# Performance work log

Hardware: AMD Instinct MI355X
Metric: run time of the kernel (lower is better)

The kernel has to match this reference:

```python
import jax, jax.numpy as jnp
import numpy as np

NEG_SLOPE = 0.2  # PyG GATv2Conv default negative_slope
NUM_GRAPHS = 512


def _gatv2_layer(x, Wl, Wr, att, bias, src, dst, n):
    # GATv2: e_ij = att . LeakyReLU(Wl x_j + Wr x_i); softmax over incoming edges of i
    xl = x @ Wl                      # [N, H] source transform
    xr = x @ Wr                      # [N, H] target transform
    e = jax.nn.leaky_relu(xl[src] + xr[dst], NEG_SLOPE)  # [E, H]
    logits = e @ att                 # [E]
    m = jax.ops.segment_max(logits, dst, num_segments=n)
    a = jnp.exp(logits - m[dst])
    denom = jax.ops.segment_sum(a, dst, num_segments=n)
    a = a / denom[dst]               # segment softmax (every node has a self loop)
    out = jax.ops.segment_sum(a[:, None] * xl[src], dst, num_segments=n)
    return out + bias


def setup_inputs() -> dict:
    key = jax.random.key(0)
    ks = jax.random.split(key, 12)
    N, E, Cin, H, Cout = 100000, 3200000, 19, 32, 4
    x = jax.random.normal(ks[0], (N, Cin), dtype=jnp.float32)
    edge_index = jax.random.randint(ks[1], (2, E), 0, N, dtype=jnp.int64)
    batch = jnp.sort(jax.random.randint(ks[2], (N,), 0, NUM_GRAPHS, dtype=jnp.int64))
    s = 0.1
    return {
        "x": x,
        "edge_index": edge_index,
        "batch": batch,
        "Wl1": jax.random.normal(ks[3], (Cin, H), dtype=jnp.float32) * s,
        "Wr1": jax.random.normal(ks[4], (Cin, H), dtype=jnp.float32) * s,
        "att1": jax.random.normal(ks[5], (H,), dtype=jnp.float32) * s,
        "b1": jnp.zeros((H,), dtype=jnp.float32),
        "Wl2": jax.random.normal(ks[6], (H, H), dtype=jnp.float32) * s,
        "Wr2": jax.random.normal(ks[7], (H, H), dtype=jnp.float32) * s,
        "att2": jax.random.normal(ks[8], (H,), dtype=jnp.float32) * s,
        "b2": jnp.zeros((H,), dtype=jnp.float32),
        "Wlin": jax.random.normal(ks[9], (H, Cout), dtype=jnp.float32) * s,
        "blin": jnp.zeros((Cout,), dtype=jnp.float32),
    }


def reference(x, edge_index, batch, Wl1, Wr1, att1, b1, Wl2, Wr2, att2, b2, Wlin, blin):
    n = x.shape[0]
    loops = jnp.arange(n, dtype=edge_index.dtype)  # add_self_loops=True (PyG default)
    src = jnp.concatenate([edge_index[0], loops])
    dst = jnp.concatenate([edge_index[1], loops])
    h = jax.nn.relu(_gatv2_layer(x, Wl1, Wr1, att1, b1, src, dst, n))
    h = jax.nn.relu(_gatv2_layer(h, Wl2, Wr2, att2, b2, src, dst, n))
    # global_mean_pool over graph ids
    sums = jax.ops.segment_sum(h, batch, num_segments=NUM_GRAPHS)
    cnt = jax.ops.segment_sum(jnp.ones((n,), h.dtype), batch, num_segments=NUM_GRAPHS)
    features = sums / jnp.maximum(cnt, 1.0)[:, None]
    logits = features @ Wlin + blin
    return logits, features
```

## Files before the change

kernel.cpp:

```cpp
#include <hip/hip_runtime.h>
#include <cstdint>
#include <cstddef>

#define WG 256
#define NPB 256
#define NPB_SHIFT 8
#define CAP 9216
#define BIN_CHUNK 4096
#define LIN_NPB 128

typedef _Float16 half4 __attribute__((ext_vector_type(4)));


__device__ __forceinline__ void lin_block(const float* __restrict__ x,
                                          const float* __restrict__ Wl,
                                          const float* __restrict__ Wr,
                                          _Float16* __restrict__ xl,
                                          _Float16* __restrict__ xr,
                                          long base_n, int N, int Cin, int t,
                                          float* sl, float* sr,
                                          float* sx0, float* sx1) {
    for (int i = t; i < Cin * 32; i += 512) { sl[i] = Wl[i]; sr[i] = Wr[i]; }
    {
        int cnt0 = (int)min((long)16, (long)N - base_n);
        if (cnt0 > 0)
            for (int i = t; i < cnt0 * Cin; i += 512)
                sx0[i] = x[base_n * Cin + i];
    }
    __syncthreads();
#pragma unroll 1
    for (int g = 0; g < LIN_NPB / 16; g++) {
        long n0 = base_n + (long)g * 16;
        if (n0 >= N) break;
        float* scur = (g & 1) ? sx1 : sx0;
        float* snxt = (g & 1) ? sx0 : sx1;
        long n1 = n0 + 16;
        if (g < LIN_NPB / 16 - 1 && n1 < N) {
            int cnt1 = (int)min((long)16, (long)N - n1);
            for (int i = t; i < cnt1 * Cin; i += 512)
                snxt[i] = x[n1 * Cin + i];
        }
        int cnt = (int)min((long)16, (long)N - n0);
        int n = t >> 5, h = t & 31;
        if (n < cnt) {
            float al = 0.f, ar = 0.f;
            for (int k = 0; k < Cin; k++) {
                float xv = scur[n * Cin + k];
                al = fmaf(xv, sl[k * 32 + h], al);
                ar = fmaf(xv, sr[k * 32 + h], ar);
            }
            xl[(n0 + n) * 32 + h] = (_Float16)al;
            xr[(n0 + n) * 32 + h] = (_Float16)ar;
        }
        __syncthreads();
    }
}

__global__ __launch_bounds__(512) void k_front(
        const int* __restrict__ esrc, const int* __restrict__ edst,
        int* __restrict__ gcnt, unsigned* __restrict__ staging,
        int E, int NB, int binBlocks,
        const float* __restrict__ x, const float* __restrict__ Wl,
        const float* __restrict__ Wr, _Float16* __restrict__ xl,
        _Float16* __restrict__ xr, int N, int Cin, int linBlocks,
        const int* __restrict__ batch, int* __restrict__ gstart, int G) {
    __shared__ unsigned sval[BIN_CHUNK];
    __shared__ unsigned short sbkt[BIN_CHUNK];
    __shared__ int hist[512];
    __shared__ int cursor[512];
    __shared__ int gbase[512];
    __shared__ int wtot[8];
    __shared__ int stotal;

    int t = threadIdx.x;

    if (blockIdx.x < (unsigned)binBlocks) {
        hist[t] = 0;
        __syncthreads();
        long base = (long)blockIdx.x * BIN_CHUNK;
        int vb[BIN_CHUNK / 512];
        unsigned vv[BIN_CHUNK / 512];
#pragma unroll
        for (int k = 0; k < BIN_CHUNK / 512; k++) {
            long e = base + k * 512 + t;
            int b = -1; unsigned v = 0;
            if (e < E) {
                int d = edst[e];
                b = d >> NPB_SHIFT;
                v = ((unsigned)esrc[e] << NPB_SHIFT) | (unsigned)(d & (NPB - 1));
                atomicAdd(&hist[b], 1);
            }
            vb[k] = b; vv[k] = v;
        }
        __syncthreads();
        int lane = t & 63, wvq = t >> 6;
        int c = hist[t];
        int v = c;
#pragma unroll
        for (int off = 1; off < 64; off <<= 1) {
            int u = __shfl_up(v, off);
            if (lane >= off) v += u;
        }
        if (lane == 63) wtot[wvq] = v;
        __syncthreads();
        int add = 0;
#pragma unroll
        for (int wq = 0; wq < 8; wq++) add += (wq < wvq) ? wtot[wq] : 0;
        int incl = v + add;
        int st = incl - c;
        cursor[t] = st;
        if (t == 511) stotal = incl;
        int wb = 0;
        if (t < NB && c > 0) wb = atomicAdd(&gcnt[t], c);
        gbase[t] = wb + t * CAP - st;
        __syncthreads();
#pragma unroll
        for (int k = 0; k < BIN_CHUNK / 512; k++) {
            int b = vb[k];
            if (b >= 0) {
                int r = atomicAdd(&cursor[b], 1);
                sval[r] = vv[k];
                sbkt[r] = (unsigned short)b;
            }
        }
        __syncthreads();
        int total = stotal;
        for (int j = t; j < total; j += 512) {
            int b = sbkt[j];
            int addr = gbase[b] + j;
            if (addr < (b + 1) * CAP)
                staging[addr] = sval[j];
        }
    } else if (blockIdx.x < (unsigned)(binBlocks + linBlocks)) {
        float* sl  = (float*)sval;
        float* sr  = (float*)sval + 1024;
        float* sx0 = (float*)sval + 2048;
        float* sx1 = sx0 + 16 * Cin;
        long base_n = (long)(blockIdx.x - binBlocks) * LIN_NPB;
        lin_block(x, Wl, Wr, xl, xr, base_n, N, Cin, t, sl, sr, sx0, sx1);
    } else {
        int g = (blockIdx.x - binBlocks - linBlocks) * 512 + t;
        if (g <= G) {
            int lo = 0, hi = N;
            while (lo < hi) {
                int mid = (lo + hi) >> 1;
                if (batch[mid] < g) lo = mid + 1; else hi = mid;
            }
            gstart[g] = lo;
        }
    }
}

__global__ __launch_bounds__(512) void k_bucket(const unsigned* __restrict__ staging,
                                                const int* __restrict__ gcnt,
                                                int* __restrict__ offsets,
                                                int* __restrict__ csr_src,
                                                int N, int NB) {
    __shared__ unsigned sslab[CAP];
    __shared__ int hist[NPB];
    __shared__ int cur[NPB];
    __shared__ int wtot[8];
    int b = blockIdx.x;
    int t = threadIdx.x;
    int lane = t & 63, wv = t >> 6;

    int a = 0;
    for (int j = t; j < b; j += 512)
        a += min(gcnt[j], CAP) + min(NPB, N - j * NPB);
#pragma unroll
    for (int off = 1; off < 64; off <<= 1) a += __shfl_xor(a, off);
    if (lane == 0) wtot[wv] = a;
    if (t < NPB) hist[t] = 0;
    __syncthreads();
    int bbase = wtot[0] + wtot[1] + wtot[2] + wtot[3]
              + wtot[4] + wtot[5] + wtot[6] + wtot[7];

    int cnt = min(gcnt[b], CAP);
    const unsigned* slab = staging + (long)b * CAP;
    for (int j = t; j < cnt; j += 512) {
        unsigned e = slab[j];
        sslab[j] = e;
        atomicAdd(&hist[e & (NPB - 1)], 1);
    }
    if (b == NB - 1 && t == 0)
        offsets[N] = bbase + cnt + min(NPB, N - b * NPB);
    __syncthreads();

    int node = b * NPB + t;
    int c = 0, v = 0;
    if (t < NPB) {
        c = (node < N) ? hist[t] + 1 : 0;
        v = c;
#pragma unroll
        for (int off = 1; off < 64; off <<= 1) {
            int u = __shfl_up(v, off);
            if (lane >= off) v += u;
        }
        if (lane == 63) wtot[wv] = v;
    }
    __syncthreads();
    if (t < NPB) {
        int add = (wv >= 1 ? wtot[0] : 0) + (wv >= 2 ? wtot[1] : 0)
                + (wv >= 3 ? wtot[2] : 0);
        int o = bbase + (v + add) - c;
        if (node < N) {
            offsets[node] = o;
            csr_src[o] = node;
            cur[t] = o + 1;
        }
    }
    __syncthreads();
    for (int j = t; j < cnt; j += 512) {
        unsigned e = sslab[j];
        int p = atomicAdd(&cur[e & (NPB - 1)], 1);
        csr_src[p] = (int)(e >> NPB_SHIFT);
    }
}

__global__ __launch_bounds__(512) void k_lin(const float* __restrict__ x,
                                             const float* __restrict__ Wl,
                                             const float* __restrict__ Wr,
                                             _Float16* __restrict__ xl,
                                             _Float16* __restrict__ xr,
                                             int N, int Cin) {
    __shared__ float sl[1024];
    __shared__ float sr[1024];
    __shared__ float sx[2][512];
    long base_n = (long)blockIdx.x * LIN_NPB;
    lin_block(x, Wl, Wr, xl, xr, base_n, N, Cin, threadIdx.x,
              sl, sr, sx[0], sx[1]);
}

__global__ __launch_bounds__(WG) void k_gat(
        const _Float16* __restrict__ xl, const _Float16* __restrict__ xr,
        const int* __restrict__ offsets, const int* __restrict__ csr,
        const float* __restrict__ att, const float* __restrict__ bias,
        float* __restrict__ out, int N) {
    int lane = threadIdx.x & 63;
    int wid = blockIdx.x * (WG / 64) + (threadIdx.x >> 6);
    int iA = wid * 2;
    if (iA >= N) return;
    int iB = iA + 1;
    int e8 = lane >> 3;
    int hq = lane & 7;
    unsigned hq8 = (unsigned)hq << 3;

    const char* xlb = (const char*)xl;
    const char* csrb = (const char*)csr;

    int startA = offsets[iA], endA = offsets[iA + 1];
    int startB = 0, endB = 0;
    if (iB < N) { startB = endA; endB = offsets[iB + 1]; }

    float4 att4 = *(const float4*)(att + hq * 4);
    const float L2E = 1.4426950408889634f;
    att4.x *= L2E; att4.y *= L2E; att4.z *= L2E; att4.w *= L2E;

    const _Float16 ns = (_Float16)0.2f;
    half4 hzero = {(_Float16)0.f, (_Float16)0.f, (_Float16)0.f, (_Float16)0.f};

    half4 xrA = *(const half4*)(xr + (long)iA * 32 + hq * 4);
    half4 xrB = hzero;
    if (iB < N) xrB = *(const half4*)(xr + (long)iB * 32 + hq * 4);

    float denomA = 0.f, denomB = 0.f;
    float4 accA = {0.f, 0.f, 0.f, 0.f};
    float4 accB = {0.f, 0.f, 0.f, 0.f};

    int itA = (endA - startA + 7) >> 3;
    int itB = (endB - startB + 7) >> 3;
    int iters = max(itA, itB);

    int pA = startA + e8, pB = startB + e8;
    int sA = -1, sB = -1;
    if (pA < endA) sA = *(const int*)(csrb + ((unsigned)pA << 2));
    if (pB < endB) sB = *(const int*)(csrb + ((unsigned)pB << 2));

    for (int it = 0; it < iters; ++it) {
        half4 xa = hzero;
        half4 xb = hzero;
        if (sA >= 0) xa = *(const half4*)(xlb + (((unsigned)sA << 6) | hq8));
        if (sB >= 0) xb = *(const half4*)(xlb + (((unsigned)sB << 6) | hq8));
        pA += 8; pB += 8;
        int sA2 = -1, sB2 = -1;
        if (pA < endA) sA2 = *(const int*)(csrb + ((unsigned)pA << 2));
        if (pB < endB) sB2 = *(const int*)(csrb + ((unsigned)pB << 2));

        {
            half4 s = xa + xrA;
            half4 m = s * ns;
            half4 tt = __builtin_elementwise_max(s, m);
            float l = fmaf((float)tt[0], att4.x,
                      fmaf((float)tt[1], att4.y,
                      fmaf((float)tt[2], att4.z,
                           (float)tt[3] * att4.w)));
            l += __shfl_xor(l, 1);
            l += __shfl_xor(l, 2);
            l += __shfl_xor(l, 4);
            float wA = __builtin_amdgcn_exp2f(l);
            wA = (sA >= 0) ? wA : 0.f;
            denomA += wA;
            accA.x = fmaf(wA, (float)xa[0], accA.x);
            accA.y = fmaf(wA, (float)xa[1], accA.y);
            accA.z = fmaf(wA, (float)xa[2], accA.z);
            accA.w = fmaf(wA, (float)xa[3], accA.w);
        }
        {
            half4 s = xb + xrB;
            half4 m = s * ns;
            half4 tt = __builtin_elementwise_max(s, m);
            float l = fmaf((float)tt[0], att4.x,
                      fmaf((float)tt[1], att4.y,
                      fmaf((float)tt[2], att4.z,
                           (float)tt[3] * att4.w)));
            l += __shfl_xor(l, 1);
            l += __shfl_xor(l, 2);
            l += __shfl_xor(l, 4);
            float wB = __builtin_amdgcn_exp2f(l);
            wB = (sB >= 0) ? wB : 0.f;
            denomB += wB;
            accB.x = fmaf(wB, (float)xb[0], accB.x);
            accB.y = fmaf(wB, (float)xb[1], accB.y);
            accB.z = fmaf(wB, (float)xb[2], accB.z);
            accB.w = fmaf(wB, (float)xb[3], accB.w);
        }
        sA = sA2; sB = sB2;
    }

    denomA += __shfl_xor(denomA, 8); denomA += __shfl_xor(denomA, 16); denomA += __shfl_xor(denomA, 32);
    denomB += __shfl_xor(denomB, 8); denomB += __shfl_xor(denomB, 16); denomB += __shfl_xor(denomB, 32);
    accA.x += __shfl_xor(accA.x, 8); accA.x += __shfl_xor(accA.x, 16); accA.x += __shfl_xor(accA.x, 32);
    accA.y += __shfl_xor(accA.y, 8); accA.y += __shfl_xor(accA.y, 16); accA.y += __shfl_xor(accA.y, 32);
    accA.z += __shfl_xor(accA.z, 8); accA.z += __shfl_xor(accA.z, 16); accA.z += __shfl_xor(accA.z, 32);
    accA.w += __shfl_xor(accA.w, 8); accA.w += __shfl_xor(accA.w, 16); accA.w += __shfl_xor(accA.w, 32);
    accB.x += __shfl_xor(accB.x, 8); accB.x += __shfl_xor(accB.x, 16); accB.x += __shfl_xor(accB.x, 32);
    accB.y += __shfl_xor(accB.y, 8); accB.y += __shfl_xor(accB.y, 16); accB.y += __shfl_xor(accB.y, 32);
    accB.z += __shfl_xor(accB.z, 8); accB.z += __shfl_xor(accB.z, 16); accB.z += __shfl_xor(accB.z, 32);
    accB.w += __shfl_xor(accB.w, 8); accB.w += __shfl_xor(accB.w, 16); accB.w += __shfl_xor(accB.w, 32);

    const float4 b4 = *(const float4*)(bias + hq * 4);
    if (lane < 8) {
        float inv = 1.0f / denomA;
        float4 o;
        o.x = fmaxf(fmaf(accA.x, inv, b4.x), 0.f);
        o.y = fmaxf(fmaf(accA.y, inv, b4.y), 0.f);
        o.z = fmaxf(fmaf(accA.z, inv, b4.z), 0.f);
        o.w = fmaxf(fmaf(accA.w, inv, b4.w), 0.f);
        *(float4*)(out + (long)iA * 32 + hq * 4) = o;
    } else if (lane < 16 && iB < N) {
        float inv = 1.0f / denomB;
        float4 o;
        o.x = fmaxf(fmaf(accB.x, inv, b4.x), 0.f);
        o.y = fmaxf(fmaf(accB.y, inv, b4.y), 0.f);
        o.z = fmaxf(fmaf(accB.z, inv, b4.z), 0.f);
        o.w = fmaxf(fmaf(accB.w, inv, b4.w), 0.f);
        *(float4*)(out + (long)iB * 32 + hq * 4) = o;
    }
}

__global__ __launch_bounds__(WG) void k_pool(const float* __restrict__ h2v,
                                             const int* __restrict__ gstart,
                                             const float* __restrict__ Wlin,
                                             const float* __restrict__ blin,
                                             float* __restrict__ out, int G) {
    __shared__ float red[WG];
    int g = blockIdx.x;
    int t = threadIdx.x;
    int h = t & 31;
    int grp = t >> 5;
    int s = gstart[g], e = gstart[g + 1];
    float acc = 0.f;
    for (int n = s + grp; n < e; n += 8)
        acc += h2v[(long)n * 32 + h];
    red[t] = acc;
    __syncthreads();
    if (grp == 0) {
        float a = red[h] + red[h + 32] + red[h + 64] + red[h + 96]
                + red[h + 128] + red[h + 160] + red[h + 192] + red[h + 224];
        int cnt = e - s;
        float c = (float)(cnt > 1 ? cnt : 1);
        float f = a / c;
        out[G * 4 + g * 32 + h] = f;
        float p0 = f * Wlin[h * 4 + 0];
        float p1 = f * Wlin[h * 4 + 1];
        float p2 = f * Wlin[h * 4 + 2];
        float p3 = f * Wlin[h * 4 + 3];
        for (int off = 1; off < 32; off <<= 1) {
            p0 += __shfl_xor(p0, off);
            p1 += __shfl_xor(p1, off);
            p2 += __shfl_xor(p2, off);
            p3 += __shfl_xor(p3, off);
        }
        if (h == 0) {
            out[g * 4 + 0] = p0 + blin[0];
            out[g * 4 + 1] = p1 + blin[1];
            out[g * 4 + 2] = p2 + blin[2];
            out[g * 4 + 3] = p3 + blin[3];
        }
    }
}

extern "C" void kernel_launch(void* const* d_in, const int* in_sizes, int n_in,
                              void* d_out, int out_size, void* d_ws, size_t ws_size,
                              hipStream_t stream) {
    const float* x    = (const float*)d_in[0];
    const int*   ei   = (const int*)d_in[1];
    const int*   batch= (const int*)d_in[2];
    const float* Wl1  = (const float*)d_in[3];
    const float* Wr1  = (const float*)d_in[4];
    const float* att1 = (const float*)d_in[5];
    const float* b1   = (const float*)d_in[6];
    const float* Wl2  = (const float*)d_in[7];
    const float* Wr2  = (const float*)d_in[8];
    const float* att2 = (const float*)d_in[9];
    const float* b2   = (const float*)d_in[10];
    const float* Wlin = (const float*)d_in[11];
    const float* blin = (const float*)d_in[12];
    float* out = (float*)d_out;

    const int N   = in_sizes[2];
    const int Cin = in_sizes[0] / N;
    const int E   = in_sizes[1] / 2;
    const int G   = out_size / 36;
    const int* src = ei;
    const int* dst = ei + E;
    const int NB  = (N + NPB - 1) >> NPB_SHIFT;

    char* w = (char*)d_ws;
    auto alloc = [&](size_t bytes) {
        char* p = w;
        w += (bytes + 255) & ~(size_t)255;
        return p;
    };
    int* offsets = (int*)alloc((size_t)(N + 1) * 4);
    int* gstart  = (int*)alloc((size_t)(G + 1) * 4);
    int* gcnt    = (int*)alloc((size_t)NB * 4);
    int* csr_src = (int*)alloc((size_t)(E + N) * 4);
    unsigned* staging = (unsigned*)alloc((size_t)NB * CAP * 4);
    _Float16* xl = (_Float16*)alloc((size_t)N * 32 * 2);
    _Float16* xr = (_Float16*)alloc((size_t)N * 32 * 2);
    float* h1    = (float*)alloc((size_t)N * 32 * 4);
    float* h2v   = h1;

    hipMemsetAsync(gcnt, 0, (size_t)NB * 4, stream);

    int binBlocks = (E + BIN_CHUNK - 1) / BIN_CHUNK;
    int linBlocks = (N + LIN_NPB - 1) / LIN_NPB;
    int stBlocks  = (G + 1 + 511) / 512;

    k_front<<<binBlocks + linBlocks + stBlocks, 512, 0, stream>>>(
        src, dst, gcnt, staging, E, NB, binBlocks,
        x, Wl1, Wr1, xl, xr, N, Cin, linBlocks,
        batch, gstart, G);

    k_bucket<<<NB, 512, 0, stream>>>(staging, gcnt, offsets, csr_src, N, NB);

    int waves = (N + 1) / 2;
    int gat_grid = (waves + 3) / 4;

    k_gat<<<gat_grid, WG, 0, stream>>>(xl, xr, offsets, csr_src, att1, b1, h1, N);

    k_lin<<<linBlocks, 512, 0, stream>>>(h1, Wl2, Wr2, xl, xr, N, 32);
    k_gat<<<gat_grid, WG, 0, stream>>>(xl, xr, offsets, csr_src, att2, b2, h2v, N);

    k_pool<<<G, WG, 0, stream>>>(h2v, gstart, Wlin, blin, out, G);
}
```

Measured before the change: 292.0 us.

## Fuse layer-2 linear transform into GAT epilogue and pooling into second GAT

The first GAT kernel now computes the layer-2 Wl/Wr projections directly from its per-node outputs using wave shuffles, removing the h1 write/read and the separate k_lin launch. The second GAT kernel accumulates mean-pooled features per graph with atomic adds, replacing the pool kernel's re-read of h2, and a small head kernel applies the final linear layer. This adds global atomics that contend on 512 graph slots, makes the float summation order nondeterministic, and reads the weight matrices from global memory inside the epilogue. The memset is widened to also zero the feature buffer.

```diff
diff --git a/kernel.cpp b/kernel.cpp
--- a/kernel.cpp
+++ b/kernel.cpp
@@ -217,25 +217,16 @@
     }
 }
 
-__global__ __launch_bounds__(512) void k_lin(const float* __restrict__ x,
-                                             const float* __restrict__ Wl,
-                                             const float* __restrict__ Wr,
-                                             _Float16* __restrict__ xl,
-                                             _Float16* __restrict__ xr,
-                                             int N, int Cin) {
-    __shared__ float sl[1024];
-    __shared__ float sr[1024];
-    __shared__ float sx[2][512];
-    long base_n = (long)blockIdx.x * LIN_NPB;
-    lin_block(x, Wl, Wr, xl, xr, base_n, N, Cin, threadIdx.x,
-              sl, sr, sx[0], sx[1]);
-}
-
+template <int MODE>
 __global__ __launch_bounds__(WG) void k_gat(
         const _Float16* __restrict__ xl, const _Float16* __restrict__ xr,
         const int* __restrict__ offsets, const int* __restrict__ csr,
         const float* __restrict__ att, const float* __restrict__ bias,
-        float* __restrict__ out, int N) {
+        int N,
+        const float* __restrict__ W2l, const float* __restrict__ W2r,
+        _Float16* __restrict__ oxl, _Float16* __restrict__ oxr,
+        const int* __restrict__ batch, const int* __restrict__ gstart,
+        float* __restrict__ feat) {
     int lane = threadIdx.x & 63;
     int wid = blockIdx.x * (WG / 64) + (threadIdx.x >> 6);
     int iA = wid * 2;
@@ -339,64 +330,85 @@
     accB.w += __shfl_xor(accB.w, 8); accB.w += __shfl_xor(accB.w, 16); accB.w += __shfl_xor(accB.w, 32);
 
     const float4 b4 = *(const float4*)(bias + hq * 4);
-    if (lane < 8) {
-        float inv = 1.0f / denomA;
-        float4 o;
-        o.x = fmaxf(fmaf(accA.x, inv, b4.x), 0.f);
-        o.y = fmaxf(fmaf(accA.y, inv, b4.y), 0.f);
-        o.z = fmaxf(fmaf(accA.z, inv, b4.z), 0.f);
-        o.w = fmaxf(fmaf(accA.w, inv, b4.w), 0.f);
-        *(float4*)(out + (long)iA * 32 + hq * 4) = o;
-    } else if (lane < 16 && iB < N) {
-        float inv = 1.0f / denomB;
-        float4 o;
-        o.x = fmaxf(fmaf(accB.x, inv, b4.x), 0.f);
-        o.y = fmaxf(fmaf(accB.y, inv, b4.y), 0.f);
-        o.z = fmaxf(fmaf(accB.z, inv, b4.z), 0.f);
-        o.w = fmaxf(fmaf(accB.w, inv, b4.w), 0.f);
-        *(float4*)(out + (long)iB * 32 + hq * 4) = o;
-    }
-}
-
-__global__ __launch_bounds__(WG) void k_pool(const float* __restrict__ h2v,
-                                             const int* __restrict__ gstart,
+    float invA = 1.0f / denomA;
+    float4 oA;
+    oA.x = fmaxf(fmaf(accA.x, invA, b4.x), 0.f);
+    oA.y = fmaxf(fmaf(accA.y, invA, b4.y), 0.f);
+    oA.z = fmaxf(fmaf(accA.z, invA, b4.z), 0.f);
+    oA.w = fmaxf(fmaf(accA.w, invA, b4.w), 0.f);
+    float4 oB = {0.f, 0.f, 0.f, 0.f};
+    if (iB < N) {
+        float invB = 1.0f / denomB;
+        oB.x = fmaxf(fmaf(accB.x, invB, b4.x), 0.f);
+        oB.y = fmaxf(fmaf(accB.y, invB, b4.y), 0.f);
+        oB.z = fmaxf(fmaf(accB.z, invB, b4.z), 0.f);
+        oB.w = fmaxf(fmaf(accB.w, invB, b4.w), 0.f);
+    }
+
+    if (MODE == 0) {
+        float oAc[4] = {oA.x, oA.y, oA.z, oA.w};
+        float oBc[4] = {oB.x, oB.y, oB.z, oB.w};
+        int hcol = lane & 31;
+        bool isB = lane >= 32;
+        float al = 0.f, ar = 0.f;
+#pragma unroll
+        for (int k = 0; k < 32; k++) {
+            float ra = __shfl(oAc[k & 3], k >> 2);
+            float rb = __shfl(oBc[k & 3], k >> 2);
+            float r = isB ? rb : ra;
+            al = fmaf(r, W2l[k * 32 + hcol], al);
+            ar = fmaf(r, W2r[k * 32 + hcol], ar);
+        }
+        long nn = isB ? (long)iB : (long)iA;
+        if (!isB || iB < N) {
+            oxl[nn * 32 + hcol] = (_Float16)al;
+            oxr[nn * 32 + hcol] = (_Float16)ar;
+        }
+    } else {
+        if (lane < 8) {
+            int g = batch[iA];
+            float rc = 1.0f / (float)max(gstart[g + 1] - gstart[g], 1);
+            atomicAdd(&feat[g * 32 + hq * 4 + 0], oA.x * rc);
+            atomicAdd(&feat[g * 32 + hq * 4 + 1], oA.y * rc);
+            atomicAdd(&feat[g * 32 + hq * 4 + 2], oA.z * rc);
+            atomicAdd(&feat[g * 32 + hq * 4 + 3], oA.w * rc);
+        } else if (lane < 16 && iB < N) {
+            int g = batch[iB];
+            float rc = 1.0f / (float)max(gstart[g + 1] - gstart[g], 1);
+            atomicAdd(&feat[g * 32 + hq * 4 + 0], oB.x * rc);
+            atomicAdd(&feat[g * 32 + hq * 4 + 1], oB.y * rc);
+            atomicAdd(&feat[g * 32 + hq * 4 + 2], oB.z * rc);
+            atomicAdd(&feat[g * 32 + hq * 4 + 3], oB.w * rc);
+        }
+    }
+}
+
+__global__ __launch_bounds__(WG) void k_head(const float* __restrict__ feat,
                                              const float* __restrict__ Wlin,
                                              const float* __restrict__ blin,
                                              float* __restrict__ out, int G) {
-    __shared__ float red[WG];
-    int g = blockIdx.x;
     int t = threadIdx.x;
     int h = t & 31;
     int grp = t >> 5;
-    int s = gstart[g], e = gstart[g + 1];
-    float acc = 0.f;
-    for (int n = s + grp; n < e; n += 8)
-        acc += h2v[(long)n * 32 + h];
-    red[t] = acc;
-    __syncthreads();
-    if (grp == 0) {
-        float a = red[h] + red[h + 32] + red[h + 64] + red[h + 96]
-                + red[h + 128] + red[h + 160] + red[h + 192] + red[h + 224];
-        int cnt = e - s;
-        float c = (float)(cnt > 1 ? cnt : 1);
-        float f = a / c;
-        out[G * 4 + g * 32 + h] = f;
-        float p0 = f * Wlin[h * 4 + 0];
-        float p1 = f * Wlin[h * 4 + 1];
-        float p2 = f * Wlin[h * 4 + 2];
-        float p3 = f * Wlin[h * 4 + 3];
-        for (int off = 1; off < 32; off <<= 1) {
-            p0 += __shfl_xor(p0, off);
-            p1 += __shfl_xor(p1, off);
-            p2 += __shfl_xor(p2, off);
-            p3 += __shfl_xor(p3, off);
-        }
-        if (h == 0) {
-            out[g * 4 + 0] = p0 + blin[0];
-            out[g * 4 + 1] = p1 + blin[1];
-            out[g * 4 + 2] = p2 + blin[2];
-            out[g * 4 + 3] = p3 + blin[3];
-        }
+    int g = blockIdx.x * 8 + grp;
+    if (g >= G) return;
+    float f = feat[g * 32 + h];
+    out[G * 4 + g * 32 + h] = f;
+    float p0 = f * Wlin[h * 4 + 0];
+    float p1 = f * Wlin[h * 4 + 1];
+    float p2 = f * Wlin[h * 4 + 2];
+    float p3 = f * Wlin[h * 4 + 3];
+    for (int off = 1; off < 32; off <<= 1) {
+        p0 += __shfl_xor(p0, off);
+        p1 += __shfl_xor(p1, off);
+        p2 += __shfl_xor(p2, off);
+        p3 += __shfl_xor(p3, off);
+    }
+    if (h == 0) {
+        out[g * 4 + 0] = p0 + blin[0];
+        out[g * 4 + 1] = p1 + blin[1];
+        out[g * 4 + 2] = p2 + blin[2];
+        out[g * 4 + 3] = p3 + blin[3];
     }
 }
 
@@ -435,14 +447,17 @@
     int* offsets = (int*)alloc((size_t)(N + 1) * 4);
     int* gstart  = (int*)alloc((size_t)(G + 1) * 4);
     int* gcnt    = (int*)alloc((size_t)NB * 4);
+    float* feat  = (float*)alloc((size_t)G * 32 * 4);
     int* csr_src = (int*)alloc((size_t)(E + N) * 4);
     unsigned* staging = (unsigned*)alloc((size_t)NB * CAP * 4);
-    _Float16* xl = (_Float16*)alloc((size_t)N * 32 * 2);
-    _Float16* xr = (_Float16*)alloc((size_t)N * 32 * 2);
-    float* h1    = (float*)alloc((size_t)N * 32 * 4);
-    float* h2v   = h1;
-
-    hipMemsetAsync(gcnt, 0, (size_t)NB * 4, stream);
+    _Float16* xl  = (_Float16*)alloc((size_t)N * 32 * 2);
+    _Float16* xr  = (_Float16*)alloc((size_t)N * 32 * 2);
+    _Float16* xl2 = (_Float16*)alloc((size_t)N * 32 * 2);
+    _Float16* xr2 = (_Float16*)alloc((size_t)N * 32 * 2);
+
+    hipMemsetAsync(gcnt, 0,
+                   (size_t)((char*)feat - (char*)gcnt) + (size_t)G * 32 * 4,
+                   stream);
 
     int binBlocks = (E + BIN_CHUNK - 1) / BIN_CHUNK;
     int linBlocks = (N + LIN_NPB - 1) / LIN_NPB;
@@ -458,10 +473,13 @@
     int waves = (N + 1) / 2;
     int gat_grid = (waves + 3) / 4;
 
-    k_gat<<<gat_grid, WG, 0, stream>>>(xl, xr, offsets, csr_src, att1, b1, h1, N);
-
-    k_lin<<<linBlocks, 512, 0, stream>>>(h1, Wl2, Wr2, xl, xr, N, 32);
-    k_gat<<<gat_grid, WG, 0, stream>>>(xl, xr, offsets, csr_src, att2, b2, h2v, N);
-
-    k_pool<<<G, WG, 0, stream>>>(h2v, gstart, Wlin, blin, out, G);
-}
+    k_gat<0><<<gat_grid, WG, 0, stream>>>(xl, xr, offsets, csr_src, att1, b1,
+                                          N, Wl2, Wr2, xl2, xr2,
+                                          nullptr, nullptr, nullptr);
+
+    k_gat<1><<<gat_grid, WG, 0, stream>>>(xl2, xr2, offsets, csr_src, att2, b2,
+                                          N, nullptr, nullptr, nullptr, nullptr,
+                                          batch, gstart, feat);
+
+    k_head<<<(G + 7) / 8, WG, 0, stream>>>(feat, Wlin, blin, out, G);
+}
```

New measurement: 366.6 us. +25.6%, slower.
